# Performance work log

Measured on AMD Instinct MI355X. Metric: run time of the kernel, lower is better.

The kernel has to match this reference:

```python
import jax, jax.numpy as jnp
import numpy as np
import math

D = 256      # d_model == channels
H = 8        # nhead
DEP = D // H # depth = 32
FF = 1024    # dim_feedforward
P = 81       # 9x9 shogi board tokens
EPS = 1e-5


def setup_inputs() -> dict:
    key = jax.random.key(0)
    ks = jax.random.split(key, 8)
    B = 2048
    x = jax.random.normal(ks[0], (B, D, 9, 9), dtype=jnp.float32)
    s = 0.02
    return {
        "x": x,
        "qkv_w": jax.random.normal(ks[1], (3 * D, D // H), dtype=jnp.float32) * s,  # grouped 1x1 conv weight
        "rel_w1": jax.random.normal(ks[2], (32, D * P), dtype=jnp.float32) * s,
        "rel_w2": jax.random.normal(ks[3], (DEP * P, 32), dtype=jnp.float32) * s,
        "o_w": jax.random.normal(ks[4], (D, D), dtype=jnp.float32) * s,
        "ff_w1": jax.random.normal(ks[5], (FF, D), dtype=jnp.float32) * s,
        "ff_w2": jax.random.normal(ks[6], (D, FF), dtype=jnp.float32) * s,
        "bn1_g": jnp.ones((D,), jnp.float32),
        "bn1_b": jnp.zeros((D,), jnp.float32),
        "bn2_g": jnp.ones((D,), jnp.float32),
        "bn2_b": jnp.zeros((D,), jnp.float32),
    }


def _batchnorm(x, g, b):
    # training-mode BN: per-channel batch stats over (B, H, W), biased variance
    mean = jnp.mean(x, axis=(0, 2, 3), keepdims=True)
    var = jnp.var(x, axis=(0, 2, 3), keepdims=True)
    return (x - mean) * jax.lax.rsqrt(var + EPS) * g[None, :, None, None] + b[None, :, None, None]


def reference(x, qkv_w, rel_w1, rel_w2, o_w, ff_w1, ff_w2, bn1_g, bn1_b, bn2_g, bn2_b):
    B = x.shape[0]
    # grouped 1x1 conv QKV: group g maps its D//H input channels to 3*DEP outputs
    xg = x.reshape(B, H, D // H, P)                      # [B, H, D/H, 81]
    wg = qkv_w.reshape(H, 3 * DEP, D // H)               # [H, 3*DEP, D/H]
    qkv = jnp.einsum('goi,bgip->bgop', wg, xg).reshape(B, 3 * D, P)
    q = qkv[:, :D].reshape(B, H, DEP, P).transpose(0, 1, 3, 2)       # [B,H,81,DEP]
    k = qkv[:, D:2 * D].reshape(B, H, DEP, P)                        # [B,H,DEP,81]
    v = qkv[:, 2 * D:].reshape(B, H, DEP, P).transpose(0, 1, 3, 2)   # [B,H,81,DEP]
    # learned relative-position bias from the whole board state
    r = (x.reshape(B, -1) @ rel_w1.T) @ rel_w2.T          # [B, DEP*81]
    r = r.reshape(B, 1, DEP, P)                           # broadcast over heads
    scores = (q @ k + q @ r) / math.sqrt(DEP)             # [B,H,81,81]
    aw = jax.nn.softmax(scores, axis=-1)
    att = (aw @ v).transpose(0, 1, 3, 2).reshape(B, D, 9, 9)
    att = jnp.einsum('oc,bchw->bohw', o_w, att)           # 1x1 output projection
    x1 = _batchnorm(att + x, bn1_g, bn1_b)
    ff = jax.nn.gelu(jnp.einsum('fc,bchw->bfhw', ff_w1, x1), approximate=False)
    ff = jnp.einsum('cf,bfhw->bchw', ff_w2, ff)
    return _batchnorm(ff + x1, bn2_g, bn2_b)
```

## Files before the change

### kernel.cpp

```cpp
#include <hip/hip_runtime.h>
#include <math.h>

#define B_   2048
#define D_   256
#define H_   8
#define DEP_ 32
#define P_   81
#define FF_  1024
#define CHW  (D_*P_)
#define NPOS (B_*P_)
#define KREL (D_*P_)
#define NTOT (B_*CHW)
#define EPS_ 1e-5f
#define YTP  264
#define YTSZ (96*YTP)

typedef __attribute__((ext_vector_type(8))) short short8v;
typedef __attribute__((ext_vector_type(4))) short short4v;
typedef __attribute__((ext_vector_type(4))) float f32x4;

__device__ __forceinline__ float bf2f(unsigned short u){
    return __uint_as_float(((unsigned int)u) << 16);
}
__device__ __forceinline__ unsigned short f2bf(float f){
    unsigned int x = __float_as_uint(f);
    return (unsigned short)((x + 0x7FFFu + ((x >> 16) & 1u)) >> 16);
}
__device__ __forceinline__ float fast_gelu(float x){
    float u = 0.70710678118654752f * x;
    float a = fabsf(u);
    float t = __builtin_amdgcn_rcpf(fmaf(0.3275911f, a, 1.f));
    float p = t * fmaf(t, fmaf(t, fmaf(t, fmaf(t, 1.061405429f, -1.453152027f),
                         1.421413741f), -0.284496736f), 0.254829592f);
    float e = __expf(-u * u);
    float er = copysignf(fmaf(-p, e, 1.f), u);
    return 0.5f * x * (1.f + er);
}
__device__ __forceinline__ float wave16_red(float v){
    v += __shfl_xor(v, 1); v += __shfl_xor(v, 2);
    v += __shfl_xor(v, 4); v += __shfl_xor(v, 8);
    return v;
}
__device__ __forceinline__ short8v frag_redist(const f32x4 c0, const f32x4 c1, int lr, int lh){
    short8v o;
    #pragma unroll
    for (int j = 0; j < 8; ++j){
        int src = lr + 16 * (2 * (lh & 1) + (j >> 2));
        float v0 = __shfl(c0[j & 3], src);
        float v1 = __shfl(c1[j & 3], src);
        o[j] = (short)f2bf(lh < 2 ? v0 : v1);
    }
    return o;
}

__global__ __launch_bounds__(256) void k_f2bf(const float* __restrict__ w,
                                              unsigned short* __restrict__ o, int n){
    int i = blockIdx.x * 256 + threadIdx.x;
    int st = gridDim.x * 256;
    for (; i < n; i += st) o[i] = f2bf(w[i]);
}

__global__ __launch_bounds__(256) void k_h_mfma(const float* __restrict__ x,
                                                const unsigned short* __restrict__ w1b,
                                                float* __restrict__ ph){
    const int bt = blockIdx.x >> 2, ks = blockIdx.x & 3;
    const int t = threadIdx.x, w = t >> 6, lane = t & 63;
    const int lr = lane & 15, lh = lane >> 4;
    const int b0 = bt * 16;
    f32x4 acc0 = {0.f,0.f,0.f,0.f}, acc1 = {0.f,0.f,0.f,0.f};
    const float* xrow = x + (size_t)(b0 + lr) * KREL;
    const unsigned short* wr0 = w1b + (size_t)lr * KREL;
    const unsigned short* wr1 = w1b + (size_t)(16 + lr) * KREL;
    for (int kk = w; kk < 162; kk += 4){
        const int k0 = (ks * 162 + kk) * 32 + lh * 8;
        short8v a0 = *(const short8v*)(wr0 + k0);
        short8v a1 = *(const short8v*)(wr1 + k0);
        const float4 xv0 = *(const float4*)(xrow + k0);
        const float4 xv1 = *(const float4*)(xrow + k0 + 4);
        short8v bb;
        bb[0] = (short)f2bf(xv0.x); bb[1] = (short)f2bf(xv0.y);
        bb[2] = (short)f2bf(xv0.z); bb[3] = (short)f2bf(xv0.w);
        bb[4] = (short)f2bf(xv1.x); bb[5] = (short)f2bf(xv1.y);
        bb[6] = (short)f2bf(xv1.z); bb[7] = (short)f2bf(xv1.w);
        acc0 = __builtin_amdgcn_mfma_f32_16x16x32_bf16(a0, bb, acc0, 0, 0, 0);
        acc1 = __builtin_amdgcn_mfma_f32_16x16x32_bf16(a1, bb, acc1, 0, 0, 0);
    }
    __shared__ float red[4][32][17];
    #pragma unroll
    for (int r = 0; r < 4; ++r){
        red[w][lh * 4 + r][lr]      = acc0[r];
        red[w][16 + lh * 4 + r][lr] = acc1[r];
    }
    __syncthreads();
    for (int i = t; i < 512; i += 256){
        int j = i >> 4, bb2 = i & 15;
        float s = red[0][j][bb2] + red[1][j][bb2] + red[2][j][bb2] + red[3][j][bb2];
        ph[(size_t)ks * 65536 + (size_t)(b0 + bb2) * 32 + j] = s;
    }
}

__global__ __launch_bounds__(256) void k_h_red(const float* __restrict__ ph,
                                               float* __restrict__ h){
    int i = blockIdx.x * 256 + threadIdx.x;
    h[i] = ph[i] + ph[65536 + i] + ph[131072 + i] + ph[196608 + i];
}

__global__ __launch_bounds__(512, 2) void k_attn_oproj8(const float* __restrict__ x,
                                                        const unsigned short* __restrict__ qkvwb,
                                                        const float* __restrict__ relw2,
                                                        const float* __restrict__ h,
                                                        const unsigned short* __restrict__ owb,
                                                        unsigned short* __restrict__ yT,
                                                        float* __restrict__ p1){
    const int b = blockIdx.x, t = threadIdx.x;
    const int lane = t & 63, w = t >> 6;
    const int lr = lane & 15, lh = lane >> 4;

    __shared__ __align__(16) unsigned short x1s[96 * 264];
    __shared__ __align__(16) unsigned short Rl[96 * 40];
    __shared__ __align__(16) unsigned short vL[8][32 * 104];
    __shared__ __align__(16) unsigned short pL[8][16 * 104];

    const float* xb = x + (size_t)b * CHW;

    {
        const float* hb = h + b * 32;
        float hreg[32];
        #pragma unroll
        for (int j = 0; j < 32; ++j) hreg[j] = hb[j];
        for (int idx = t; idx < 2592; idx += 512){
            int d = idx / 81, p = idx - d * 81;
            const float4* wr = (const float4*)(relw2 + (size_t)idx * 32);
            float s = 0.f;
            #pragma unroll
            for (int j = 0; j < 8; ++j){
                float4 wv = wr[j];
                s += wv.x * hreg[4*j] + wv.y * hreg[4*j+1] + wv.z * hreg[4*j+2] + wv.w * hreg[4*j+3];
            }
            Rl[p * 40 + d] = f2bf(s);
        }
        for (int idx = t; idx < 15 * 32; idx += 512){
            int p = 81 + (idx >> 5), d = idx & 31;
            Rl[p * 40 + d] = 0;
        }
    }
    for (int idx = t; idx < 15 * 132; idx += 512){
        int r = idx / 132, c = idx - r * 132;
        *(unsigned int*)&x1s[(81 + r) * 264 + 2 * c] = 0;
    }
    {
        float* tb = (float*)vL;
        for (int cc = 0; cc < 4; ++cc){
            for (int idx = t; idx < 64 * 81; idx += 512){
                int c = idx / 81, p = idx - c * 81;
                tb[c * 85 + p] = xb[(cc * 64 + c) * 81 + p];
            }
            __syncthreads();
            for (int idx = t; idx < 32 * 81; idx += 512){
                int c2 = idx & 31, p = idx >> 5;
                int c = 2 * c2;
                unsigned int pk = (unsigned int)f2bf(tb[c * 85 + p])
                                | ((unsigned int)f2bf(tb[(c + 1) * 85 + p]) << 16);
                *(unsigned int*)&x1s[p * 264 + cc * 64 + c] = pk;
            }
            __syncthreads();
        }
    }

    const int hh = w;
    const int qrow = hh * 32, krow = 256 + hh * 32, vrow = 512 + hh * 32;
    const int gq = (qrow / 96) * 32, gk = (krow / 96) * 32, gv = (vrow / 96) * 32;
    unsigned short* v_ = vL[w];
    unsigned short* p_ = pL[w];

    short8v bqf[6];
    {
        short8v a0 = *(const short8v*)(qkvwb + (size_t)(qrow + lr) * 32 + lh * 8);
        short8v a1 = *(const short8v*)(qkvwb + (size_t)(qrow + 16 + lr) * 32 + lh * 8);
        #pragma unroll
        for (int nt = 0; nt < 6; ++nt){
            short8v bb = *(const short8v*)(x1s + (nt * 16 + lr) * 264 + gq + lh * 8);
            f32x4 c0 = {0.f,0.f,0.f,0.f}, c1 = {0.f,0.f,0.f,0.f};
            c0 = __builtin_amdgcn_mfma_f32_16x16x32_bf16(a0, bb, c0, 0, 0, 0);
            c1 = __builtin_amdgcn_mfma_f32_16x16x32_bf16(a1, bb, c1, 0, 0, 0);
            bqf[nt] = frag_redist(c0, c1, lr, lh);
        }
    }
    short8v akf[6];
    {
        short8v a0 = *(const short8v*)(qkvwb + (size_t)(krow + lr) * 32 + lh * 8);
        short8v a1 = *(const short8v*)(qkvwb + (size_t)(krow + 16 + lr) * 32 + lh * 8);
        #pragma unroll
        for (int mt = 0; mt < 6; ++mt){
            int p = mt * 16 + lr;
            short4v r0 = *(const short4v*)(Rl + p * 40 + lh * 4);
            short4v r1 = *(const short4v*)(Rl + p * 40 + 16 + lh * 4);
            f32x4 c0, c1;
            #pragma unroll
            for (int r = 0; r < 4; ++r){
                c0[r] = bf2f((unsigned short)r0[r]);
                c1[r] = bf2f((unsigned short)r1[r]);
            }
            short8v bb = *(const short8v*)(x1s + p * 264 + gk + lh * 8);
            c0 = __builtin_amdgcn_mfma_f32_16x16x32_bf16(a0, bb, c0, 0, 0, 0);
            c1 = __builtin_amdgcn_mfma_f32_16x16x32_bf16(a1, bb, c1, 0, 0, 0);
            akf[mt] = frag_redist(c0, c1, lr, lh);
        }
    }
    {
        short8v a0 = *(const short8v*)(qkvwb + (size_t)(vrow + lr) * 32 + lh * 8);
        short8v a1 = *(const short8v*)(qkvwb + (size_t)(vrow + 16 + lr) * 32 + lh * 8);
        #pragma unroll
        for (int nt = 0; nt < 6; ++nt){
            short8v bb = *(const short8v*)(x1s + (nt * 16 + lr) * 264 + gv + lh * 8);
            f32x4 c0 = {0.f,0.f,0.f,0.f}, c1 = {0.f,0.f,0.f,0.f};
            c0 = __builtin_amdgcn_mfma_f32_16x16x32_bf16(a0, bb, c0, 0, 0, 0);
            c1 = __builtin_amdgcn_mfma_f32_16x16x32_bf16(a1, bb, c1, 0, 0, 0);
            int pk = nt * 16 + lr;
            #pragma unroll
            for (int r = 0; r < 4; ++r){
                v_[(lh * 4 + r) * 104 + pk]      = f2bf(c0[r]);
                v_[(16 + lh * 4 + r) * 104 + pk] = f2bf(c1[r]);
            }
        }
    }

    f32x4 oA[6], oB[6];
    #pragma unroll
    for (int nt = 0; nt < 6; ++nt){
        f32x4 sc[6];
        #pragma unroll
        for (int mt = 0; mt < 6; ++mt){
            f32x4 z = {0.f,0.f,0.f,0.f};
            sc[mt] = __builtin_amdgcn_mfma_f32_16x16x32_bf16(akf[mt], bqf[nt], z, 0, 0, 0);
        }
        sc[5][0] = (lh == 0) ? sc[5][0] : -1e30f;
        sc[5][1] = -1e30f; sc[5][2] = -1e30f; sc[5][3] = -1e30f;
        float mx = -1e30f;
        #pragma unroll
        for (int mt = 0; mt < 6; ++mt)
        #pragma unroll
        for (int r = 0; r < 4; ++r) mx = fmaxf(mx, sc[mt][r]);
        mx = fmaxf(mx, __shfl_xor(mx, 16));
        mx = fmaxf(mx, __shfl_xor(mx, 32));
        const float scl = 0.17677669529663687f;
        float sum = 0.f;
        #pragma unroll
        for (int mt = 0; mt < 6; ++mt)
        #pragma unroll
        for (int r = 0; r < 4; ++r){
            float e = __expf((sc[mt][r] - mx) * scl);
            sc[mt][r] = e; sum += e;
        }
        sum += __shfl_xor(sum, 16);
        sum += __shfl_xor(sum, 32);
        float inv = 1.f / sum;
        #pragma unroll
        for (int mt = 0; mt < 6; ++mt){
            short4v pv;
            #pragma unroll
            for (int r = 0; r < 4; ++r) pv[r] = (short)f2bf(sc[mt][r] * inv);
            *(short4v*)(p_ + lr * 104 + mt * 16 + lh * 4) = pv;
        }
        f32x4 o0 = {0.f,0.f,0.f,0.f}, o1 = {0.f,0.f,0.f,0.f};
        #pragma unroll
        for (int ks = 0; ks < 3; ++ks){
            short8v ap  = *(const short8v*)(p_ + lr * 104 + ks * 32 + lh * 8);
            short8v bv0 = *(const short8v*)(v_ + lr * 104 + ks * 32 + lh * 8);
            short8v bv1 = *(const short8v*)(v_ + (16 + lr) * 104 + ks * 32 + lh * 8);
            o0 = __builtin_amdgcn_mfma_f32_16x16x32_bf16(ap, bv0, o0, 0, 0, 0);
            o1 = __builtin_amdgcn_mfma_f32_16x16x32_bf16(ap, bv1, o1, 0, 0, 0);
        }
        oA[nt] = o0;
        oB[nt] = o1;
    }

    __syncthreads();
    #pragma unroll
    for (int nt = 0; nt < 6; ++nt){
        #pragma unroll
        for (int r = 0; r < 4; ++r){
            int pq = nt * 16 + lh * 4 + r;
            if (pq < 81){
                x1s[pq * 264 + hh * 32 + lr]      = f2bf(oA[nt][r]);
                x1s[pq * 264 + hh * 32 + 16 + lr] = f2bf(oB[nt][r]);
            }
        }
    }
    __syncthreads();

    const int cw = w * 32;
    f32x4 acc[2][6];
    #pragma unroll
    for (int ci = 0; ci < 2; ++ci)
    #pragma unroll
    for (int pj = 0; pj < 6; ++pj)
        acc[ci][pj] = (f32x4){0.f, 0.f, 0.f, 0.f};

    for (int ks = 0; ks < 8; ++ks){
        const int k0 = ks * 32 + lh * 8;
        short8v a[2];
        #pragma unroll
        for (int ci = 0; ci < 2; ++ci)
            a[ci] = *(const short8v*)(owb + (size_t)(cw + ci * 16 + lr) * 256 + k0);
        #pragma unroll
        for (int pj = 0; pj < 6; ++pj){
            short8v bb = *(const short8v*)(x1s + (pj * 16 + lr) * 264 + k0);
            #pragma unroll
            for (int ci = 0; ci < 2; ++ci)
                acc[ci][pj] = __builtin_amdgcn_mfma_f32_16x16x32_bf16(a[ci], bb, acc[ci][pj], 0, 0, 0);
        }
    }
    unsigned short* yb = yT + (size_t)b * YTSZ;
    float cs[8], cq[8];
    #pragma unroll
    for (int i = 0; i < 8; ++i){ cs[i] = 0.f; cq[i] = 0.f; }
    #pragma unroll
    for (int ci = 0; ci < 2; ++ci)
    #pragma unroll
    for (int pj = 0; pj < 6; ++pj){
        int p = pj * 16 + lr;
        int c = cw + ci * 16 + lh * 4;
        short4v pk;
        if (p < 81){
            #pragma unroll
            for (int r = 0; r < 4; ++r){
                float y = acc[ci][pj][r] + xb[(c + r) * 81 + p];
                pk[r] = (short)f2bf(y);
                cs[ci * 4 + r] += y;
                cq[ci * 4 + r] += y * y;
            }
        } else {
            #pragma unroll
            for (int r = 0; r < 4; ++r) pk[r] = 0;
        }
        *(short4v*)(yb + p * YTP + c) = pk;
    }
    #pragma unroll
    for (int i = 0; i < 8; ++i){
        cs[i] = wave16_red(cs[i]);
        cq[i] = wave16_red(cq[i]);
    }
    if (lr == 0){
        #pragma unroll
        for (int ci = 0; ci < 2; ++ci)
        #pragma unroll
        for (int r = 0; r < 4; ++r){
            int c = cw + ci * 16 + lh * 4 + r;
            p1[(size_t)c * 2048 + b]         = cs[ci * 4 + r];
            p1[(size_t)(256 + c) * 2048 + b] = cq[ci * 4 + r];
        }
    }
}

__global__ __launch_bounds__(256) void k_red(const float* __restrict__ part,
                                             const float* __restrict__ g, const float* __restrict__ bia,
                                             float* __restrict__ sOut, float* __restrict__ tOut){
    const int c = blockIdx.x, t = threadIdx.x;
    float s = 0.f, q = 0.f;
    #pragma unroll
    for (int i = 0; i < 8; ++i){
        s += part[(size_t)c * 2048 + t + i * 256];
        q += part[(size_t)(256 + c) * 2048 + t + i * 256];
    }
    __shared__ float rs[256], rq[256];
    rs[t] = s; rq[t] = q;
    __syncthreads();
    for (int k = 128; k; k >>= 1){
        if (t < k){ rs[t] += rs[t + k]; rq[t] += rq[t + k]; }
        __syncthreads();
    }
    if (t == 0){
        float m = rs[0] / (float)NPOS;
        float var = rq[0] / (float)NPOS - m * m;
        float sc = g[c] * rsqrtf(var + EPS_);
        sOut[c] = sc;
        tOut[c] = bia[c] - m * sc;
    }
}

__global__ __launch_bounds__(256) void k_w1scale(const float* __restrict__ w1,
                                                 const float* __restrict__ s1,
                                                 unsigned short* __restrict__ w1s){
    const int f = blockIdx.x, t = threadIdx.x;
    w1s[f * 256 + t] = f2bf(w1[f * 256 + t] * s1[t]);
}

__global__ __launch_bounds__(64) void k_bias1(const float* __restrict__ w1,
                                              const float* __restrict__ t1,
                                              float* __restrict__ bias1){
    const int f = blockIdx.x, t = threadIdx.x;
    const float4 wv = *(const float4*)(w1 + f * 256 + t * 4);
    const float4 tv = *(const float4*)(t1 + t * 4);
    float s = wv.x * tv.x + wv.y * tv.y + wv.z * tv.z + wv.w * tv.w;
    #pragma unroll
    for (int m = 1; m < 64; m <<= 1) s += __shfl_xor(s, m);
    if (t == 0) bias1[f] = s;
}

__global__ __launch_bounds__(256, 2) void k_ff_v4(unsigned short* __restrict__ yT,
                                                  const unsigned short* __restrict__ w1s,
                                                  const unsigned short* __restrict__ w2bf,
                                                  const float* __restrict__ bias1,
                                                  const float* __restrict__ s1, const float* __restrict__ t1,
                                                  float* __restrict__ p2){
    const int b = blockIdx.x, t = threadIdx.x;
    const int lane = t & 63, w = t >> 6;
    const int lr = lane & 15, lh = lane >> 4;

    __shared__ __align__(16) unsigned short x1s[96 * 264];
    __shared__ __align__(16) unsigned short ffs[2][96 * 72];

    {
        const short8v* src = (const short8v*)(yT + (size_t)b * YTSZ);
        short8v* dst = (short8v*)x1s;
        for (int idx = t; idx < 3168; idx += 256) dst[idx] = src[idx];
    }
    __syncthreads();

    const int cw = w * 64;
    const int fl = w * 16 + lh * 4;
    f32x4 acc2[4][6];
    #pragma unroll
    for (int ci = 0; ci < 4; ++ci)
    #pragma unroll
    for (int pj = 0; pj < 6; ++pj)
        acc2[ci][pj] = (f32x4){0.f, 0.f, 0.f, 0.f};

    auto g1_kloop = [&](int fc, f32x4 (&acc1)[6]){
        const int fbase = fc * 64 + w * 16;
        float b4[4];
        #pragma unroll
        for (int r = 0; r < 4; ++r) b4[r] = bias1[fbase + lh * 4 + r];
        #pragma unroll
        for (int pj = 0; pj < 6; ++pj){
            acc1[pj][0] = b4[0]; acc1[pj][1] = b4[1];
            acc1[pj][2] = b4[2]; acc1[pj][3] = b4[3];
        }
        #pragma unroll
        for (int ks = 0; ks < 8; ++ks){
            const int k0 = ks * 32 + lh * 8;
            short8v a0 = *(const short8v*)(w1s + (size_t)(fbase + lr) * 256 + k0);
            #pragma unroll
            for (int pj = 0; pj < 6; ++pj){
                short8v bb = *(const short8v*)(x1s + (pj * 16 + lr) * 264 + k0);
                acc1[pj] = __builtin_amdgcn_mfma_f32_16x16x32_bf16(a0, bb, acc1[pj], 0, 0, 0);
            }
        }
    };
    auto g2 = [&](int fc, int bf){
        #pragma unroll
        for (int ks2 = 0; ks2 < 2; ++ks2){
            const int k0 = ks2 * 32 + lh * 8;
            short8v a2[4];
            #pragma unroll
            for (int ci = 0; ci < 4; ++ci)
                a2[ci] = *(const short8v*)(w2bf + (size_t)(cw + ci * 16 + lr) * 1024 + fc * 64 + k0);
            #pragma unroll
            for (int pj = 0; pj < 6; ++pj){
                short8v bb = *(const short8v*)(ffs[bf] + (pj * 16 + lr) * 72 + k0);
                #pragma unroll
                for (int ci = 0; ci < 4; ++ci)
                    acc2[ci][pj] = __builtin_amdgcn_mfma_f32_16x16x32_bf16(a2[ci], bb, acc2[ci][pj], 0, 0, 0);
            }
        }
    };
    auto gelu_store = [&](const f32x4 (&acc1)[6], int bf){
        #pragma unroll
        for (int pj = 0; pj < 6; ++pj){
            int p = pj * 16 + lr;
            short4v pk;
            #pragma unroll
            for (int r = 0; r < 4; ++r)
                pk[r] = (short)f2bf(fast_gelu(acc1[pj][r]));
            *(short4v*)&ffs[bf][p * 72 + fl] = pk;
        }
    };

    {
        f32x4 acc1[6];
        g1_kloop(0, acc1);
        gelu_store(acc1, 0);
    }
    __syncthreads();
    for (int fc = 0; fc < 15; ++fc){
        f32x4 acc1[6];
        g1_kloop(fc + 1, acc1);
        g2(fc, fc & 1);
        gelu_store(acc1, (fc + 1) & 1);
        __syncthreads();
    }
    g2(15, 1);

    float sv[16], tv[16];
    #pragma unroll
    for (int ci = 0; ci < 4; ++ci)
    #pragma unroll
    for (int r = 0; r < 4; ++r){
        int c = cw + ci * 16 + lh * 4 + r;
        sv[ci * 4 + r] = s1[c];
        tv[ci * 4 + r] = t1[c];
    }
    unsigned short* zb = yT + (size_t)b * YTSZ;
    float cs[16], cq[16];
    #pragma unroll
    for (int i = 0; i < 16; ++i){ cs[i] = 0.f; cq[i] = 0.f; }
    #pragma unroll
    for (int ci = 0; ci < 4; ++ci)
    #pragma unroll
    for (int pj = 0; pj < 6; ++pj){
        int p = pj * 16 + lr;
        if (p < 81){
            int c = cw + ci * 16 + lh * 4;
            short4v yv = *(const short4v*)&x1s[p * 264 + c];
            short4v pk;
            #pragma unroll
            for (int r = 0; r < 4; ++r){
                float x1 = fmaf(bf2f((unsigned short)yv[r]), sv[ci * 4 + r], tv[ci * 4 + r]);
                float z = acc2[ci][pj][r] + x1;
                pk[r] = (short)f2bf(z);
                cs[ci * 4 + r] += z;
                cq[ci * 4 + r] += z * z;
            }
            *(short4v*)(zb + p * YTP + c) = pk;
        }
    }
    #pragma unroll
    for (int i = 0; i < 16; ++i){
        cs[i] = wave16_red(cs[i]);
        cq[i] = wave16_red(cq[i]);
    }
    if (lr == 0){
        #pragma unroll
        for (int ci = 0; ci < 4; ++ci)
        #pragma unroll
        for (int r = 0; r < 4; ++r){
            int c = cw + ci * 16 + lh * 4 + r;
            p2[(size_t)c * 2048 + b]         = cs[ci * 4 + r];
            p2[(size_t)(256 + c) * 2048 + b] = cq[ci * 4 + r];
        }
    }
}

__global__ __launch_bounds__(256) void k_bnapply_t(const unsigned short* __restrict__ yTz,
                                                   const float* __restrict__ s2, const float* __restrict__ t2,
                                                   float* __restrict__ out){
    const int b = blockIdx.x, t = threadIdx.x;
    __shared__ __align__(16) unsigned short zs[96 * 264];
    __shared__ float s2s[256], t2s[256];
    s2s[t] = s2[t];
    t2s[t] = t2[t];
    {
        const short8v* src = (const short8v*)(yTz + (size_t)b * YTSZ);
        short8v* dst = (short8v*)zs;
        for (int idx = t; idx < 3168; idx += 256) dst[idx] = src[idx];
    }
    __syncthreads();
    float* ob = out + (size_t)b * CHW;
    for (int idx = t; idx < CHW; idx += 256){
        int c = idx / 81, p = idx - c * 81;
        ob[idx] = fmaf(bf2f(zs[p * 264 + c]), s2s[c], t2s[c]);
    }
}

extern "C" void kernel_launch(void* const* d_in, const int* in_sizes, int n_in,
                              void* d_out, int out_size, void* d_ws, size_t ws_size,
                              hipStream_t stream){
    const float* x     = (const float*)d_in[0];
    const float* qkvw  = (const float*)d_in[1];
    const float* relw1 = (const float*)d_in[2];
    const float* relw2 = (const float*)d_in[3];
    const float* ow    = (const float*)d_in[4];
    const float* ffw1  = (const float*)d_in[5];
    const float* ffw2  = (const float*)d_in[6];
    const float* g1    = (const float*)d_in[7];
    const float* b1    = (const float*)d_in[8];
    const float* g2    = (const float*)d_in[9];
    const float* b2    = (const float*)d_in[10];
    float* out = (float*)d_out;
    char* ws = (char*)d_ws;

    unsigned short* w1rel = (unsigned short*)ws;
    float* h     = (float*)(ws + 1327104);
    unsigned short* w2bf  = (unsigned short*)(ws + 2117632);
    unsigned short* qkvwb = (unsigned short*)(ws + 2641920);
    unsigned short* owb   = (unsigned short*)(ws + 2691072);
    unsigned short* w1s   = (unsigned short*)(ws + 2822144);
    float* bias1 = (float*)(ws + 3346432);
    float* s1    = (float*)(ws + 3350528);
    float* t1    = (float*)(ws + 3351552);
    float* s2    = (float*)(ws + 3352576);
    float* t2    = (float*)(ws + 3353600);
    float* p1    = (float*)(ws + 3354624);
    float* p2    = (float*)(ws + 7548928);
    unsigned short* yT = (unsigned short*)(ws + 11743232);
    float* p_h = p1;

    hipLaunchKernelGGL(k_f2bf, dim3(1024), dim3(256), 0, stream, relw1, w1rel, 663552);
    hipLaunchKernelGGL(k_f2bf, dim3(256),  dim3(256), 0, stream, ffw2, w2bf, 262144);
    hipLaunchKernelGGL(k_f2bf, dim3(96),   dim3(256), 0, stream, qkvw, qkvwb, 24576);
    hipLaunchKernelGGL(k_f2bf, dim3(256),  dim3(256), 0, stream, ow, owb, 65536);

    hipLaunchKernelGGL(k_h_mfma, dim3(512), dim3(256), 0, stream, x, w1rel, p_h);
    hipLaunchKernelGGL(k_h_red,  dim3(256), dim3(256), 0, stream, p_h, h);
    hipLaunchKernelGGL(k_attn_oproj8, dim3(2048), dim3(512), 0, stream, x, qkvwb, relw2, h, owb, yT, p1);
    hipLaunchKernelGGL(k_red,      dim3(256),  dim3(256), 0, stream, p1, g1, b1, s1, t1);
    hipLaunchKernelGGL(k_w1scale,  dim3(1024), dim3(256), 0, stream, ffw1, s1, w1s);
    hipLaunchKernelGGL(k_bias1,    dim3(1024), dim3(64),  0, stream, ffw1, t1, bias1);
    hipLaunchKernelGGL(k_ff_v4,    dim3(2048), dim3(256), 0, stream, yT, w1s, w2bf, bias1, s1, t1, p2);
    hipLaunchKernelGGL(k_red,      dim3(256),  dim3(256), 0, stream, p2, g2, b2, s2, t2);
    hipLaunchKernelGGL(k_bnapply_t, dim3(2048), dim3(256), 0, stream, yT, s2, t2, out);
}
```

Baseline: 821.4 us.

## Split FFN kernel into two position-half blocks per sample for higher occupancy

The fused FFN kernel now launches two blocks per batch sample, each handling 48 of the 96 padded positions. This halves shared memory and accumulator registers per block, allowing up to 4 blocks per CU instead of 2. BN2 partial statistics go to two separate buffers, with p1 reused as the second one, and a new reduction kernel sums both. The cost is that each block reads the full W1/W2 weights, doubling weight traffic per sample, and the A-fragment reuse per MFMA is halved.

Result: slower. 989.1 us (+20.4%).

```diff
diff --git a/kernel.cpp b/kernel.cpp
--- a/kernel.cpp
+++ b/kernel.cpp
@@ -379,6 +379,35 @@
     }
 }
 
+__global__ __launch_bounds__(256) void k_red2(const float* __restrict__ pa,
+                                              const float* __restrict__ pb,
+                                              const float* __restrict__ g, const float* __restrict__ bia,
+                                              float* __restrict__ sOut, float* __restrict__ tOut){
+    const int c = blockIdx.x, t = threadIdx.x;
+    float s = 0.f, q = 0.f;
+    #pragma unroll
+    for (int i = 0; i < 8; ++i){
+        size_t idx = (size_t)c * 2048 + t + i * 256;
+        size_t idq = (size_t)(256 + c) * 2048 + t + i * 256;
+        s += pa[idx] + pb[idx];
+        q += pa[idq] + pb[idq];
+    }
+    __shared__ float rs[256], rq[256];
+    rs[t] = s; rq[t] = q;
+    __syncthreads();
+    for (int k = 128; k; k >>= 1){
+        if (t < k){ rs[t] += rs[t + k]; rq[t] += rq[t + k]; }
+        __syncthreads();
+    }
+    if (t == 0){
+        float m = rs[0] / (float)NPOS;
+        float var = rq[0] / (float)NPOS - m * m;
+        float sc = g[c] * rsqrtf(var + EPS_);
+        sOut[c] = sc;
+        tOut[c] = bia[c] - m * sc;
+    }
+}
+
 __global__ __launch_bounds__(256) void k_w1scale(const float* __restrict__ w1,
                                                  const float* __restrict__ s1,
                                                  unsigned short* __restrict__ w1s){
@@ -398,42 +427,44 @@
     if (t == 0) bias1[f] = s;
 }
 
-__global__ __launch_bounds__(256, 2) void k_ff_v4(unsigned short* __restrict__ yT,
+__global__ __launch_bounds__(256, 4) void k_ff_v5(unsigned short* __restrict__ yT,
                                                   const unsigned short* __restrict__ w1s,
                                                   const unsigned short* __restrict__ w2bf,
                                                   const float* __restrict__ bias1,
                                                   const float* __restrict__ s1, const float* __restrict__ t1,
-                                                  float* __restrict__ p2){
-    const int b = blockIdx.x, t = threadIdx.x;
+                                                  float* __restrict__ p2a,
+                                                  float* __restrict__ p2b){
+    const int b = blockIdx.x >> 1, hhalf = blockIdx.x & 1;
+    const int t = threadIdx.x;
     const int lane = t & 63, w = t >> 6;
     const int lr = lane & 15, lh = lane >> 4;
 
-    __shared__ __align__(16) unsigned short x1s[96 * 264];
-    __shared__ __align__(16) unsigned short ffs[2][96 * 72];
-
-    {
-        const short8v* src = (const short8v*)(yT + (size_t)b * YTSZ);
+    __shared__ __align__(16) unsigned short x1s[48 * 264];
+    __shared__ __align__(16) unsigned short ffs[2][48 * 72];
+
+    {
+        const short8v* src = (const short8v*)(yT + (size_t)b * YTSZ + hhalf * 48 * YTP);
         short8v* dst = (short8v*)x1s;
-        for (int idx = t; idx < 3168; idx += 256) dst[idx] = src[idx];
+        for (int idx = t; idx < 1584; idx += 256) dst[idx] = src[idx];
     }
     __syncthreads();
 
     const int cw = w * 64;
     const int fl = w * 16 + lh * 4;
-    f32x4 acc2[4][6];
+    f32x4 acc2[4][3];
     #pragma unroll
     for (int ci = 0; ci < 4; ++ci)
     #pragma unroll
-    for (int pj = 0; pj < 6; ++pj)
+    for (int pj = 0; pj < 3; ++pj)
         acc2[ci][pj] = (f32x4){0.f, 0.f, 0.f, 0.f};
 
-    auto g1_kloop = [&](int fc, f32x4 (&acc1)[6]){
+    auto g1_kloop = [&](int fc, f32x4 (&acc1)[3]){
         const int fbase = fc * 64 + w * 16;
         float b4[4];
         #pragma unroll
         for (int r = 0; r < 4; ++r) b4[r] = bias1[fbase + lh * 4 + r];
         #pragma unroll
-        for (int pj = 0; pj < 6; ++pj){
+        for (int pj = 0; pj < 3; ++pj){
             acc1[pj][0] = b4[0]; acc1[pj][1] = b4[1];
             acc1[pj][2] = b4[2]; acc1[pj][3] = b4[3];
         }
@@ -442,7 +473,7 @@
             const int k0 = ks * 32 + lh * 8;
             short8v a0 = *(const short8v*)(w1s + (size_t)(fbase + lr) * 256 + k0);
             #pragma unroll
-            for (int pj = 0; pj < 6; ++pj){
+            for (int pj = 0; pj < 3; ++pj){
                 short8v bb = *(const short8v*)(x1s + (pj * 16 + lr) * 264 + k0);
                 acc1[pj] = __builtin_amdgcn_mfma_f32_16x16x32_bf16(a0, bb, acc1[pj], 0, 0, 0);
             }
@@ -457,7 +488,7 @@
             for (int ci = 0; ci < 4; ++ci)
                 a2[ci] = *(const short8v*)(w2bf + (size_t)(cw + ci * 16 + lr) * 1024 + fc * 64 + k0);
             #pragma unroll
-            for (int pj = 0; pj < 6; ++pj){
+            for (int pj = 0; pj < 3; ++pj){
                 short8v bb = *(const short8v*)(ffs[bf] + (pj * 16 + lr) * 72 + k0);
                 #pragma unroll
                 for (int ci = 0; ci < 4; ++ci)
@@ -465,9 +496,9 @@
             }
         }
     };
-    auto gelu_store = [&](const f32x4 (&acc1)[6], int bf){
-        #pragma unroll
-        for (int pj = 0; pj < 6; ++pj){
+    auto gelu_store = [&](const f32x4 (&acc1)[3], int bf){
+        #pragma unroll
+        for (int pj = 0; pj < 3; ++pj){
             int p = pj * 16 + lr;
             short4v pk;
             #pragma unroll
@@ -478,13 +509,13 @@
     };
 
     {
-        f32x4 acc1[6];
+        f32x4 acc1[3];
         g1_kloop(0, acc1);
         gelu_store(acc1, 0);
     }
     __syncthreads();
     for (int fc = 0; fc < 15; ++fc){
-        f32x4 acc1[6];
+        f32x4 acc1[3];
         g1_kloop(fc + 1, acc1);
         g2(fc, fc & 1);
         gelu_store(acc1, (fc + 1) & 1);
@@ -501,18 +532,19 @@
         sv[ci * 4 + r] = s1[c];
         tv[ci * 4 + r] = t1[c];
     }
-    unsigned short* zb = yT + (size_t)b * YTSZ;
+    unsigned short* zb = yT + (size_t)b * YTSZ + hhalf * 48 * YTP;
     float cs[16], cq[16];
     #pragma unroll
     for (int i = 0; i < 16; ++i){ cs[i] = 0.f; cq[i] = 0.f; }
     #pragma unroll
     for (int ci = 0; ci < 4; ++ci)
     #pragma unroll
-    for (int pj = 0; pj < 6; ++pj){
-        int p = pj * 16 + lr;
-        if (p < 81){
+    for (int pj = 0; pj < 3; ++pj){
+        int lp = pj * 16 + lr;
+        int pg = hhalf * 48 + lp;
+        if (pg < 81){
             int c = cw + ci * 16 + lh * 4;
-            short4v yv = *(const short4v*)&x1s[p * 264 + c];
+            short4v yv = *(const short4v*)&x1s[lp * 264 + c];
             short4v pk;
             #pragma unroll
             for (int r = 0; r < 4; ++r){
@@ -522,7 +554,7 @@
                 cs[ci * 4 + r] += z;
                 cq[ci * 4 + r] += z * z;
             }
-            *(short4v*)(zb + p * YTP + c) = pk;
+            *(short4v*)(zb + lp * YTP + c) = pk;
         }
     }
     #pragma unroll
@@ -530,14 +562,15 @@
         cs[i] = wave16_red(cs[i]);
         cq[i] = wave16_red(cq[i]);
     }
+    float* pout = hhalf ? p2b : p2a;
     if (lr == 0){
         #pragma unroll
         for (int ci = 0; ci < 4; ++ci)
         #pragma unroll
         for (int r = 0; r < 4; ++r){
             int c = cw + ci * 16 + lh * 4 + r;
-            p2[(size_t)c * 2048 + b]         = cs[ci * 4 + r];
-            p2[(size_t)(256 + c) * 2048 + b] = cq[ci * 4 + r];
+            pout[(size_t)c * 2048 + b]         = cs[ci * 4 + r];
+            pout[(size_t)(256 + c) * 2048 + b] = cq[ci * 4 + r];
         }
     }
 }
@@ -607,7 +640,7 @@
     hipLaunchKernelGGL(k_red,      dim3(256),  dim3(256), 0, stream, p1, g1, b1, s1, t1);
     hipLaunchKernelGGL(k_w1scale,  dim3(1024), dim3(256), 0, stream, ffw1, s1, w1s);
     hipLaunchKernelGGL(k_bias1,    dim3(1024), dim3(64),  0, stream, ffw1, t1, bias1);
-    hipLaunchKernelGGL(k_ff_v4,    dim3(2048), dim3(256), 0, stream, yT, w1s, w2bf, bias1, s1, t1, p2);
-    hipLaunchKernelGGL(k_red,      dim3(256),  dim3(256), 0, stream, p2, g2, b2, s2, t2);
+    hipLaunchKernelGGL(k_ff_v5,    dim3(4096), dim3(256), 0, stream, yT, w1s, w2bf, bias1, s1, t1, p2, p1);
+    hipLaunchKernelGGL(k_red2,     dim3(256),  dim3(256), 0, stream, p2, p1, g2, b2, s2, t2);
     hipLaunchKernelGGL(k_bnapply_t, dim3(2048), dim3(256), 0, stream, yT, s2, t2, out);
 }
```
